# Kernel tuning notes

Measured on AMD Instinct MI355X. Metric: run time of the kernel, lower is better.

## Reference

```python
import jax, jax.numpy as jnp
from jax import lax
import numpy as np

D = 1024   # d_model
N = 64     # d_state
P = 64     # headdim
H = 16     # nheads = d_inner // headdim (d_inner = d_model)
E = 8      # n_experts
R = 8      # LoRA rank
OM = 32    # omega_dim
MEMD = 384 # memory vector dim
KC = 4     # d_conv
Bz, Lz = 2, 1024


def setup_inputs() -> dict:
    key = jax.random.key(0)
    it = iter(jax.random.split(key, 48))
    def nrm(shape, s=0.02):
        return jax.random.normal(next(it), shape, jnp.float32) * s
    return dict(
        x=jax.random.normal(next(it), (Bz, Lz, D), jnp.float32),
        wkv_state=nrm((Bz, N, N), 0.1),
        x_prev=jax.random.normal(next(it), (Bz, 1, D), jnp.float32),
        memory_vec=jax.random.normal(next(it), (Bz, MEMD), jnp.float32),
        rag_state=nrm((Bz, N, N), 0.1),
        ssd_state=nrm((Bz, H, P, N), 0.1),
        conv_state=nrm((Bz, D, KC), 0.1),
        norm_scale=jnp.ones((D,), jnp.float32), norm_bias=jnp.zeros((D,), jnp.float32),
        W_in=nrm((2 * D, D)), conv_w=nrm((D, KC), 0.1), conv_b=jnp.zeros((D,), jnp.float32),
        W_dt=nrm((H, D)), dt_bias=jnp.full((H,), -2.0, jnp.float32),
        A_log=jnp.log(jnp.linspace(0.5, 8.0, H)).astype(jnp.float32),
        W_B=nrm((N, D)), W_C=nrm((N, D)), W_ssd_out=nrm((D, D)),
        W_r=nrm((N, D)), W_k=nrm((N, D)), W_v=nrm((N, D)), W_w=nrm((N, D)),
        W_rwkv_out=nrm((D, N)),
        W_skew=nrm((OM, OM), 0.1), W_om_in=nrm((OM, D)), W_om_out=nrm((D, OM)),
        W_router=nrm((E, D)), lora_A=nrm((E, D, R)), lora_B=nrm((E, R, D)),
        W_nov=nrm((1, 2 * D)), b_nov=jnp.zeros((1,), jnp.float32),
        W_ragq=nrm((N, D)), W_rago=nrm((D, N)),
        W_mq=nrm((MEMD, D)), W_mp=nrm((D, MEMD)),
        W_mg=nrm((1, D + MEMD)), b_mg=jnp.zeros((1,), jnp.float32),
    )


def _layernorm(x, s, b):
    m = x.mean(-1, keepdims=True)
    v = ((x - m) ** 2).mean(-1, keepdims=True)
    return (x - m) * lax.rsqrt(v + 1e-5) * s + b


def _forward(x, wkv_state, x_prev, memory_vec, rag_state, ssd_state, conv_state,
             norm_scale, norm_bias, W_in, conv_w, conv_b, W_dt, dt_bias, A_log,
             W_B, W_C, W_ssd_out, W_r, W_k, W_v, W_w, W_rwkv_out,
             W_skew, W_om_in, W_om_out, W_router, lora_A, lora_B, W_nov, b_nov,
             W_ragq, W_rago, W_mq, W_mp, W_mg, b_mg):
    Bb, Ll, _ = x.shape
    residual = x
    xn = _layernorm(x, norm_scale, norm_bias)
    # ---- TarsCoreBlock: Mamba-2 SSD scan + RWKV-7 wkv scan + gated fusion ----
    zu = xn @ W_in.T
    z, u = zu[..., :D], zu[..., D:]
    # depthwise causal conv1d with rolling conv_state [B, D, KC]
    u_cat = jnp.concatenate([conv_state.transpose(0, 2, 1), u], axis=1)  # [B, KC+L, D]
    acc = conv_b
    for k in range(KC):
        acc = acc + u_cat[:, k:k + Ll, :] * conv_w[:, k]
    uc = jax.nn.silu(acc)
    conv_new = u_cat[:, Ll:, :].transpose(0, 2, 1)
    dt = jax.nn.softplus(xn @ W_dt.T + dt_bias)   # [B,L,H]
    A = -jnp.exp(A_log)                            # [H], negative decay rates
    Bm = xn @ W_B.T                                # [B,L,N]
    Cm = xn @ W_C.T                                # [B,L,N]
    uh = uc.reshape(Bb, Ll, H, P)
    def ssd_step(h, inp):
        dt_t, u_t, b_t, c_t = inp                  # [B,H],[B,H,P],[B,N],[B,N]
        h = h * jnp.exp(dt_t * A)[..., None, None] + (dt_t[..., None, None] * u_t[..., None]) * b_t[:, None, None, :]
        return h, jnp.einsum('bhpn,bn->bhp', h, c_t)
    ssd_new, ys = lax.scan(ssd_step, ssd_state,
                           (dt.transpose(1, 0, 2), uh.transpose(1, 0, 2, 3),
                            Bm.transpose(1, 0, 2), Cm.transpose(1, 0, 2)))
    y_ssd = ys.transpose(1, 0, 2, 3).reshape(Bb, Ll, D) @ W_ssd_out.T
    # RWKV-7 style wkv recurrence with time-shift mixing
    x_shift = jnp.concatenate([x_prev, xn[:, :-1]], axis=1)
    mix = 0.5 * (xn + x_shift)
    r, kk, v = mix @ W_r.T, mix @ W_k.T, mix @ W_v.T
    w = jnp.exp(-jnp.exp(mix @ W_w.T))             # per-channel decay in (0,1)
    def rwkv_step(S, inp):
        r_t, k_t, v_t, w_t = inp
        S = S * w_t[:, :, None] + v_t[:, :, None] * k_t[:, None, :]
        return S, jnp.einsum('bij,bj->bi', S, r_t)
    wkv_new, yr = lax.scan(rwkv_step, wkv_state,
                           (r.transpose(1, 0, 2), kk.transpose(1, 0, 2),
                            v.transpose(1, 0, 2), w.transpose(1, 0, 2)))
    y_rwkv = yr.transpose(1, 0, 2) @ W_rwkv_out.T
    core_out = jax.nn.silu(z) * y_ssd + y_rwkv     # WuNeng fusion
    x1 = residual + core_out
    x_prev_new = xn[:, -1:, :]
    # ---- RAG injection from compressed rag_state ----
    q = x1.mean(1) @ W_ragq.T                      # [B,N]
    info = jnp.einsum('bij,bj->bi', rag_state, q)
    x1 = x1 + 0.1 * (info @ W_rago.T)[:, None, :]
    # ---- Omega-SSM: Cayley SO(n) rotation in omega subspace ----
    Ask = 0.5 * (W_skew - W_skew.T)
    I = jnp.eye(OM, dtype=x.dtype)
    Qc = jnp.linalg.solve(I - Ask, I + Ask)        # orthogonal via Cayley map
    x1 = x1 + ((x1 @ W_om_in.T) @ Qc.T) @ W_om_out.T
    # ---- MoLE: sparse top-2 low-rank (LoRA) experts ----
    probs = jax.nn.softmax(x1 @ W_router.T, axis=-1)  # [B,L,E]
    _, topi = lax.top_k(probs, 2)
    mask = jax.nn.one_hot(topi, E, dtype=x.dtype).sum(-2)
    gate = probs * mask
    gate = gate / (gate.sum(-1, keepdims=True) + 1e-9)
    down = jnp.einsum('bld,edr->bler', x1, lora_A)    # [B,L,E,R]
    x2 = x1 + jnp.einsum('bler,erd->bld', down * gate[..., None], lora_B)
    aux = E * jnp.sum(probs.mean((0, 1)) * mask.mean((0, 1)))
    # ---- NoveltyGate blended residual ----
    h_old, h_new = residual.mean(1), x2.mean(1)
    novelty = jax.nn.sigmoid(jnp.concatenate([h_old, h_new], -1) @ W_nov.T + b_nov)[:, 0]
    n = novelty[:, None, None]
    x3 = n * x2 + (1.0 - n) * residual
    # ---- Cosine-gated memory fusion ----
    h_post = x3.mean(1)
    hq = h_post @ W_mq.T
    sim = (hq * memory_vec).sum(-1) / (jnp.linalg.norm(hq, axis=-1) * jnp.linalg.norm(memory_vec, axis=-1) + 1e-8)
    gm = jax.nn.sigmoid(jnp.concatenate([h_post, memory_vec], -1) @ W_mg.T + b_mg)[:, 0]
    x4 = x3 + (sim * gm)[:, None, None] * (memory_vec @ W_mp.T)[:, None, :]
    return x4, wkv_new, x_prev_new, ssd_new, conv_new, aux


def reference(x, wkv_state, x_prev, memory_vec, rag_state, ssd_state, conv_state,
              norm_scale, norm_bias, W_in, conv_w, conv_b, W_dt, dt_bias, A_log,
              W_B, W_C, W_ssd_out, W_r, W_k, W_v, W_w, W_rwkv_out,
              W_skew, W_om_in, W_om_out, W_router, lora_A, lora_B, W_nov, b_nov,
              W_ragq, W_rago, W_mq, W_mp, W_mg, b_mg):
    return _forward(x, wkv_state, x_prev, memory_vec, rag_state, ssd_state, conv_state,
                    norm_scale, norm_bias, W_in, conv_w, conv_b, W_dt, dt_bias, A_log,
                    W_B, W_C, W_ssd_out, W_r, W_k, W_v, W_w, W_rwkv_out,
                    W_skew, W_om_in, W_om_out, W_router, lora_A, lora_B, W_nov, b_nov,
                    W_ragq, W_rago, W_mq, W_mp, W_mg, b_mg)
```

## Files before the change

### kernel.cpp

```cpp
#include <hip/hip_runtime.h>
#include <hip/hip_bf16.h>

#define DD    1024
#define NN    64
#define HH    16
#define EE    8
#define OMM   32
#define MEMDD 384
#define BB    2
#define LL    1024
#define TT    2048

#define OFF_X4    0
#define OFF_WKV   2097152
#define OFF_XPREV 2105344
#define OFF_SSD   2107392
#define OFF_CONV  2238464
#define OFF_AUX   2246656

typedef unsigned short u16;
typedef __attribute__((ext_vector_type(8))) short short8;
typedef __attribute__((ext_vector_type(4))) float f32x4;

__device__ __forceinline__ float us2f(u16 u){ return __uint_as_float(((unsigned)u)<<16); }
// ... 216 lines not shown
        for (int n=0;n<4;++n) acc[m][n] = (f32x4){0.f,0.f,0.f,0.f};
    for (int k0=0; k0<K; k0+=64){
        #pragma unroll
        for (int i=0;i<2;++i){
            int row = wid*16 + i*8 + lr;
            gl_lds16(Ag + (size_t)row*K + k0 + lc8, &Asm[(wid*16 + i*8)*64]);
        }
        #pragma unroll
        for (int i=0;i<4;++i){
            int row = wid*32 + i*8 + lr;
            gl_lds16(Wg + (size_t)row*K + k0 + lc8, &Bsm[(wid*32 + i*8)*64]);
        }
        __syncthreads();
        #pragma unroll
        for (int ks=0; ks<2; ++ks){
            short8 af[2], bf[4];
            #pragma unroll
            for (int m=0;m<2;++m)
                af[m] = *(const short8*)&Asm[(wr*32 + m*16 + l15)*64 + ks*32 + quad*8];
            #pragma unroll
            for (int n=0;n<4;++n)
                bf[n] = *(const short8*)&Bsm[(wc*64 + n*16 + l15)*64 + ks*32 + quad*8];
            #pragma unroll
            for (int m=0;m<2;++m)
                #pragma unroll
                for (int n=0;n<4;++n)
                    acc[m][n] = __builtin_amdgcn_mfma_f32_16x16x32_bf16(af[m], bf[n], acc[m][n], 0,0,0);
        }
        __syncthreads();
    }
    int ns1 = N - Nsplit;
    #pragma unroll
    for (int m=0;m<2;++m){
        #pragma unroll
        for (int n=0;n<4;++n){
            int col = bn + wc*64 + n*16 + l15;
            #pragma unroll
            for (int i=0;i<4;++i){
                int row = bm + wr*32 + m*16 + quad*4 + i;
                float v = acc[m][n][i];
                if (col < Nsplit){
                    size_t id = (size_t)row*Nsplit + col;
                    if (c0bf) ((u16*)C0)[id] = f2us(v);
                    else C0[id] = (addto ? C0[id] : 0.f) + v;
                } else {
                    size_t id = (size_t)row*ns1 + (col - Nsplit);
                    C1[id] = v;
                }
            }
        }
    }
}

__global__ __launch_bounds__(256)
void gemm_big_k(const u16* __restrict__ A, const u16* __restrict__ W,
                float* __restrict__ C0, float* __restrict__ C1,
                int N, int K, int Nsplit, int addto){
    __shared__ u16 Asm[64*64];
    __shared__ u16 Bsm[128*64];
    gemm_body(Asm, Bsm, A, W, C0, C1, N, K, Nsplit, addto, 0, blockIdx.x, blockIdx.y);
}

__device__ __forceinline__ void gemm64_body(u16* Asm, u16* Bsm,
                const u16* __restrict__ A, const u16* __restrict__ W,
                float* __restrict__ C0, float* __restrict__ C1,
                int N, int K, int Nsplit, int c0bf, int bx, int by){
    int tid = threadIdx.x;
    int wid = tid >> 6, lane = tid & 63;
    int l15 = lane & 15, quad = lane >> 4;
    int wr = wid >> 1, wc = wid & 1;
    int bm = bx*64, bn = by*64;
    int lr = lane >> 3;
    int lc8 = (lane & 7)*8;
    const u16* Ag = A + (size_t)bm*K;
    const u16* Wg = W + (size_t)bn*K;
    f32x4 acc[2][2];
    #pragma unroll
    for (int m=0;m<2;++m)
        #pragma unroll
        for (int n=0;n<2;++n) acc[m][n] = (f32x4){0.f,0.f,0.f,0.f};
    for (int k0=0; k0<K; k0+=64){
        #pragma unroll
        for (int i=0;i<2;++i){
            int row = wid*16 + i*8 + lr;
            gl_lds16(Ag + (size_t)row*K + k0 + lc8, &Asm[(wid*16 + i*8)*64]);
        }
        #pragma unroll
        for (int i=0;i<2;++i){
            int row = wid*16 + i*8 + lr;
            gl_lds16(Wg + (size_t)row*K + k0 + lc8, &Bsm[(wid*16 + i*8)*64]);
        }
        __syncthreads();
        #pragma unroll
        for (int ks=0; ks<2; ++ks){
            short8 af[2], bf[2];
            #pragma unroll
            for (int m=0;m<2;++m)
                af[m] = *(const short8*)&Asm[(wr*32 + m*16 + l15)*64 + ks*32 + quad*8];
            #pragma unroll
            for (int n=0;n<2;++n)
                bf[n] = *(const short8*)&Bsm[(wc*32 + n*16 + l15)*64 + ks*32 + quad*8];
            #pragma unroll
            for (int m=0;m<2;++m)
                #pragma unroll
                for (int n=0;n<2;++n)
                    acc[m][n] = __builtin_amdgcn_mfma_f32_16x16x32_bf16(af[m], bf[n], acc[m][n], 0,0,0);
        }
        __syncthreads();
    }
    int ns1 = N - Nsplit;
    #pragma unroll
    for (int m=0;m<2;++m){
        #pragma unroll
        for (int n=0;n<2;++n){
            int col = bn + wc*32 + n*16 + l15;
// ... 84 lines not shown
                #pragma unroll
                for (int n=0;n<4;++n)
                    acc[m][n] = __builtin_amdgcn_mfma_f32_16x16x32_bf16(af[m], bf[n], acc[m][n], 0,0,0);
        }
        __syncthreads();
    }
    int ns1 = N - Nsplit;
    #pragma unroll
    for (int m=0;m<4;++m){
        #pragma unroll
        for (int n=0;n<4;++n){
            int col = bn + wc*64 + n*16 + l15;
            #pragma unroll
            for (int i=0;i<4;++i){
                int row = bm + wr*64 + m*16 + quad*4 + i;
                float v = acc[m][n][i];
                if (col < Nsplit){
                    C0[(size_t)row*Nsplit + col] = v;
                } else {
                    C1[(size_t)row*ns1 + (col - Nsplit)] = v;
                }
            }
        }
    }
}

__global__ __launch_bounds__(256)
void cmx_k(const float* __restrict__ u, const u16* __restrict__ xnbf,
           const void* __restrict__ cs, const void* __restrict__ cw, const void* __restrict__ cb,
           const void* __restrict__ xprev,
           u16* __restrict__ ucbf, u16* __restrict__ mixbf, void* __restrict__ out,
           const int* modep){
    const int m = *modep;
    int idx = blockIdx.x*256 + threadIdx.x;
    int t = idx >> 10, d = idx & 1023;
    int b = t >> 10, l = t & 1023;
    float acc = LD(cb, d, m);
    #pragma unroll
    for (int k=0;k<4;++k){
        int i = l + k;
        float xv = (i < 4) ? LD(cs, ((size_t)(b*DD + d))*4 + i, m)
                           : u[(size_t)(t + k - 4)*DD + d];
        acc += xv * LD(cw, d*4 + k, m);
    }
    ucbf[idx] = f2us(acc * sigf(acc));
    float xc = us2f(xnbf[idx]);
    float xp = (l == 0) ? LD(xprev, (size_t)b*DD + d, m) : us2f(xnbf[idx - DD]);
    mixbf[idx] = f2us(0.5f*(xc + xp));
    if (l >= LL-4)
        ST(out, OFF_CONV + (size_t)b*DD*4 + d*4 + (l - (LL-4)), u[idx], m);
}

#define LDSS 72
__global__ __launch_bounds__(256)
void ssdA_k(const u16* __restrict__ pcat2, const float* __restrict__ dtraw,
            const u16* __restrict__ ucbf,
            const void* __restrict__ A_log, const void* __restrict__ dt_bias,
            float* __restrict__ ys, float* __restrict__ Scb, float* __restrict__ cumsb,
            const int* modep){
    __shared__ u16 Bs[64*LDSS];
    __shared__ u16 Cs[64*LDSS];
    __shared__ u16 BTw[64*LDSS];
    __shared__ u16 XTs[64*LDSS];
    __shared__ float cums[64];
    __shared__ float dts_raw[64];
    const int m = *modep;
    int tid = threadIdx.x;
    int wid = tid >> 6, lane = tid & 63;
    int blk = blockIdx.x;
    int b = blk >> 8, h = (blk >> 4) & 15, c = blk & 15;
    int l16 = lane & 15, quad = lane >> 4;
    int r = tid >> 2;
    int cb4 = (tid & 3) * 16;
    float Ah = -expf(LD(A_log, h, m));
    int t0 = c*64;
    const u16* Pg = pcat2 + (size_t)(b*LL + t0)*128;
    #pragma unroll
    for (int i=0;i<4;++i){
        int cc = cb4 + i*4;
        ushort4 f = *(const ushort4*)(Pg + (size_t)r*128 + cc);
        u16* d1 = &Bs[r*LDSS + cc];
        d1[0]=f.x; d1[1]=f.y; d1[2]=f.z; d1[3]=f.w;
        ushort4 g = *(const ushort4*)(Pg + (size_t)r*128 + 64 + cc);
        u16* d2 = &Cs[r*LDSS + cc];
        d2[0]=g.x; d2[1]=g.y; d2[2]=g.z; d2[3]=g.w;
    }
    if (wid == 0){
        float raw = dtraw[(size_t)(b*LL + t0 + lane)*128 + h] + LD(dt_bias, h, m);
        float dtv = (raw > 20.f) ? raw : log1pf(expf(raw));
        dts_raw[lane] = dtv;
        float xv = dtv * Ah;
        #pragma unroll
        for (int off=1; off<64; off<<=1){
            float tu = __shfl_up(xv, off);
            if (lane >= off) xv += tu;
        }
        cums[lane] = xv;
        cumsb[(size_t)blk*64 + lane] = xv;
    }
    __syncthreads();
    float cum63 = cums[63];
    {
        float dtv = dts_raw[r];
        float wdec = expf(cum63 - cums[r]);
        const u16* ug = ucbf + (size_t)(b*LL + t0 + r)*DD + h*64;
        #pragma unroll
        for (int i=0;i<4;++i){
            int cc = cb4 + i*4;
            ushort4 f = *(const ushort4*)(ug + cc);
            XTs[(cc+0)*LDSS + r]=f2us(dtv*us2f(f.x));
            XTs[(cc+1)*LDSS + r]=f2us(dtv*us2f(f.y));
            XTs[(cc+2)*LDSS + r]=f2us(dtv*us2f(f.z));
            XTs[(cc+3)*LDSS + r]=f2us(dtv*us2f(f.w));
            u16* bsrc = &Bs[r*LDSS + cc];
            BTw[(cc+0)*LDSS + r] = f2us(us2f(bsrc[0])*wdec);
            BTw[(cc+1)*LDSS + r] = f2us(us2f(bsrc[1])*wdec);
            BTw[(cc+2)*LDSS + r] = f2us(us2f(bsrc[2])*wdec);
            BTw[(cc+3)*LDSS + r] = f2us(us2f(bsrc[3])*wdec);
        }
    }
    __syncthreads();
    f32x4 gacc[4];
    #pragma unroll
    for (int nt=0;nt<4;++nt) gacc[nt]=(f32x4){0.f,0.f,0.f,0.f};
    #pragma unroll
    for (int ks=0; ks<64; ks+=32){
        short8 af = *(const short8*)&Cs[(wid*16 + l16)*LDSS + ks + quad*8];
        #pragma unroll
        for (int nt=0;nt<4;++nt){
            short8 bf = *(const short8*)&Bs[(nt*16 + l16)*LDSS + ks + quad*8];
            gacc[nt] = __builtin_amdgcn_mfma_f32_16x16x32_bf16(af, bf, gacc[nt], 0,0,0);
        }
    }
    __syncthreads();
    #pragma unroll
    for (int nt=0;nt<4;++nt){
        int s_loc = nt*16 + l16;
        #pragma unroll
        for (int i=0;i<4;++i){
            int t_loc = wid*16 + quad*4 + i;
            float gv = (s_loc <= t_loc) ? gacc[nt][i]*expf(cums[t_loc]-cums[s_loc]) : 0.f;
            Bs[t_loc*LDSS + s_loc] = f2us(gv);
        }
    }
    __syncthreads();
    f32x4 acc2[4], acc4[4];
    #pragma unroll
    for (int nt=0;nt<4;++nt){ acc2[nt]=(f32x4){0.f,0.f,0.f,0.f}; acc4[nt]=(f32x4){0.f,0.f,0.f,0.f}; }
    #pragma unroll
    for (int ks=0; ks<64; ks+=32){
        short8 sf = *(const short8*)&Bs[(wid*16 + l16)*LDSS + ks + quad*8];
        short8 xf = *(const short8*)&XTs[(wid*16 + l16)*LDSS + ks + quad*8];
        #pragma unroll
        for (int nt=0;nt<4;++nt){
            short8 xo = *(const short8*)&XTs[(nt*16 + l16)*LDSS + ks + quad*8];
            acc2[nt] = __builtin_amdgcn_mfma_f32_16x16x32_bf16(sf, xo, acc2[nt], 0,0,0);
            short8 bo = *(const short8*)&BTw[(nt*16 + l16)*LDSS + ks + quad*8];
            acc4[nt] = __builtin_amdgcn_mfma_f32_16x16x32_bf16(xf, bo, acc4[nt], 0,0,0);
        }
    }
    #pragma unroll
    for (int nt=0;nt<4;++nt){
        int col = nt*16 + l16;
        #pragma unroll
        for (int i=0;i<4;++i){
            int row = wid*16 + quad*4 + i;
            ys[(size_t)(b*LL + t0 + row)*DD + h*64 + col] = acc2[nt][i];
            Scb[(size_t)blk*4096 + row*64 + col] = acc4[nt][i];
        }
    }
}

#define FS 68
__global__ __launch_bounds__(512)
void rwkvA_k(const float* __restrict__ rkvw,
             float* __restrict__ yr, float* __restrict__ Slb, float* __restrict__ Wcumb){
    __shared__ float wch[64*FS], vch[64*FS], kch[64*FS], rch[64*FS];
    __shared__ float Wc[64*FS];
    __shared__ float part[8*512];
    int tid = threadIdx.x;
    int wid = tid >> 6, lane = tid & 63;
    int blk = blockIdx.x;
    int b = blk >> 4, c = blk & 15;
    int t0 = c*64;
    int r = tid >> 3, c8 = (tid & 7)*8;
    const float* base = rkvw + (size_t)(b*LL + t0)*256;
    #pragma unroll
    for (int i=0;i<2;++i){
        int cc = c8 + i*4;
        *(float4*)&rch[r*FS+cc] = *(const float4*)(base + (size_t)r*256 + cc);
        *(float4*)&kch[r*FS+cc] = *(const float4*)(base + (size_t)r*256 + 64 + cc);
        *(float4*)&vch[r*FS+cc] = *(const float4*)(base + (size_t)r*256 + 128 + cc);
        float4 wv = *(const float4*)(base + (size_t)r*256 + 192 + cc);
        wch[r*FS+cc+0] = expf(-expf(wv.x));
        wch[r*FS+cc+1] = expf(-expf(wv.y));
        wch[r*FS+cc+2] = expf(-expf(wv.z));
        wch[r*FS+cc+3] = expf(-expf(wv.w));
    }
    __syncthreads();
    if (wid == 0){
        float cum = 1.f;
        for (int t=0;t<64;++t){ cum *= wch[t*FS+lane]; Wc[t*FS+lane] = cum; }
    }
    __syncthreads();
    #pragma unroll
    for (int q=0;q<8;++q){
        int idx = q*512 + tid;
        int t = idx >> 6, i = idx & 63;
        Wcumb[(size_t)blk*4096 + idx] = Wc[t*FS + i];
    }
    float S[8];
    #pragma unroll
    for (int jj=0;jj<8;++jj) S[jj]=0.f;
    int jb = wid*8;
    for (int t8=0; t8<8; ++t8){
        float ya[8];
        #pragma unroll
        for (int u=0;u<8;++u){
            int t = t8*8+u;
            float wv = wch[t*FS+lane];
            float vv = vch[t*FS+lane];
            float yy0=0.f, yy1=0.f;
            #pragma unroll
            for (int jj=0;jj<8;jj+=2){
                float k0v = kch[t*FS + jb + jj+0], r0v = rch[t*FS + jb + jj+0];
                float k1v = kch[t*FS + jb + jj+1], r1v = rch[t*FS + jb + jj+1];
                S[jj+0] = S[jj+0]*wv + vv*k0v; yy0 += S[jj+0]*r0v;
                S[jj+1] = S[jj+1]*wv + vv*k1v; yy1 += S[jj+1]*r1v;
            }
            ya[u] = yy0+yy1;
        }
        #pragma unroll
        for (int u=0;u<8;++u) part[wid*512 + u*64 + lane] = ya[u];
        __syncthreads();
        {
            int u = tid >> 6, i = tid & 63;
            float y = 0.f;
            #pragma unroll
            for (int w=0;w<8;++w) y += part[w*512 + u*64 + i];
            yr[(size_t)(b*LL + t0 + t8*8 + u)*NN + i] = y;
        }
        __syncthreads();
    }
    #pragma unroll
    for (int jj=0;jj<8;++jj)
        Slb[(size_t)blk*4096 + (size_t)lane*64 + jb + jj] = S[jj];
}

__global__ __launch_bounds__(256)
void sb_k(const void* __restrict__ ssd_state, const float* __restrict__ Scb,
          const float* __restrict__ cumsb, u16* __restrict__ hinb,
          const void* __restrict__ wkv_state, const float* __restrict__ Slb,
          const float* __restrict__ Wcumb, u16* __restrict__ hinr,
          void* __restrict__ out, const int* modep){
    const int m = *modep;
    int tid = threadIdx.x;
    if (blockIdx.x < 512){
        int bh = blockIdx.x >> 4, i = blockIdx.x & 15;
        int e = i*256 + tid;
        float h = LD(ssd_state, (size_t)bh*4096 + e, m);
        for (int c=0; c<16; ++c){
            int blk = bh*16 + c;
            float efull = expf(cumsb[(size_t)blk*64 + 63]);
            hinb[(size_t)blk*4096 + e] = f2us(h);
            h = efull*h + Scb[(size_t)blk*4096 + e];
        }
        ST(out, OFF_SSD + (size_t)bh*4096 + e, h, m);
    } else {
        int idx2 = blockIdx.x - 512;
        int b = idx2 >> 4, q = idx2 & 15;
        int e = q*256 + tid;
        int i = e >> 6;
        float S = LD(wkv_state, (size_t)b*4096 + e, m);
        for (int c=0; c<16; ++c){
            int blk = b*16 + c;
            hinr[(size_t)blk*4096 + e] = f2us(S);
            float P = Wcumb[(size_t)blk*4096 + 63*64 + i];
            S = S*P + Slb[(size_t)blk*4096 + e];
        }
        ST(out, OFF_WKV + (size_t)b*4096 + e, S, m);
    }
}

__global__ __launch_bounds__(256)
void sc_k(const u16* __restrict__ pcat2, const u16* __restrict__ hinb,
          const float* __restrict__ cumsb, const float* __restrict__ ys, u16* __restrict__ ysbf,
          const float* __restrict__ rkvw, const u16* __restrict__ hinr,
          const float* __restrict__ Wcumb, const float* __restrict__ yr, u16* __restrict__ ybf){
    __shared__ u16 T0[64*LDSS];
    __shared__ u16 T1[64*LDSS];
    int tid = threadIdx.x;
    int wid = tid >> 6, lane = tid & 63;
    int l16 = lane & 15, quad = lane >> 4;
    int r = tid >> 2;
    int cb4 = (tid & 3)*16;
    if (blockIdx.x < 512){
        int blk = blockIdx.x;
        int b = blk >> 8, h = (blk >> 4) & 15, c = blk & 15;
        int t0 = c*64;
// ... 50 lines not shown
        __syncthreads();
        f32x4 acc[4];
        #pragma unroll
        for (int nt=0;nt<4;++nt) acc[nt]=(f32x4){0.f,0.f,0.f,0.f};
        #pragma unroll
        for (int ks=0; ks<64; ks+=32){
            short8 af = *(const short8*)&T0[(wid*16 + l16)*LDSS + ks + quad*8];
            #pragma unroll
            for (int nt=0;nt<4;++nt){
                short8 hf = *(const short8*)&T1[(nt*16 + l16)*LDSS + ks + quad*8];
                acc[nt] = __builtin_amdgcn_mfma_f32_16x16x32_bf16(af, hf, acc[nt], 0,0,0);
            }
        }
        #pragma unroll
        for (int nt=0;nt<4;++nt){
            int col = nt*16 + l16;
            #pragma unroll
            for (int i=0;i<4;++i){
                int row = wid*16 + quad*4 + i;
                float Wt = Wcumb[(size_t)blk*4096 + row*64 + col];
                size_t id = (size_t)(b*LL + t0 + row)*NN + col;
                ybf[id] = f2us(yr[id] + Wt*acc[nt][i]);
            }
        }
    }
}

__global__ __launch_bounds__(256)
void fuse_mean_k(const float* __restrict__ z, const float* __restrict__ s1,
                 const float* __restrict__ s2, const void* __restrict__ xin,
                 float* __restrict__ x1, u16* __restrict__ x1bf, float* __restrict__ mean1,
                 float* __restrict__ hold, const int* modep){
    const int m = *modep;
    int bid = blockIdx.x;
    int lc = bid & 63, dc = (bid >> 6) & 3, b = bid >> 8;
    int d = dc*256 + threadIdx.x;
    float sum = 0.f, sumx = 0.f;
    int l0 = lc*16;
    for (int l=l0; l<l0+16; ++l){
        size_t idx = (size_t)(b*LL + l)*DD + d;
        float zl = z[idx];
        float xv = LD(xin, idx, m);
        float v = xv + zl*sigf(zl)*s1[idx] + s2[idx];
        x1[idx] = v;
        x1bf[idx] = f2us(v);
        sum += v;
        sumx += xv;
    }
    atomicAdd(&mean1[b*DD + d], sum*(1.f/LL));
    atomicAdd(&hold[b*DD + d], sumx*(1.f/LL));
}

__global__ __launch_bounds__(256)
void ragA_k(const float* __restrict__ mean1, const void* __restrict__ W_ragq,
            float* __restrict__ qb, const int* modep){
    const int m = *modep;
    int bx = blockIdx.x;
    int b = bx >> 4;
    int tid = threadIdx.x, wid = tid >> 6, lane = tid & 63;
    int row = (bx & 15)*4 + wid;
    float s = 0.f;
    size_t wo = (size_t)row*DD;
    #pragma unroll
    for (int it=0; it<16; ++it)
        s += LD(W_ragq, wo + it*64 + lane, m) * mean1[(b<<10) + it*64 + lane];
    s = wave_sum64(s);
    if (lane == 0) qb[b*64 + row] = s;
}

__global__ __launch_bounds__(256)
void ragB_k(const float* __restrict__ qb, const void* __restrict__ rag_state,
            float* __restrict__ infob, const int* modep){
    const int m = *modep;
    int bx = blockIdx.x;
    int b = bx >> 4;
    int tid = threadIdx.x, wid = tid >> 6, lane = tid & 63;
    int row = (bx & 15)*4 + wid;
    float s = LD(rag_state, (size_t)(b*64+row)*64 + lane, m) * qb[b*64 + lane];
    s = wave_sum64(s);
    if (lane == 0) infob[b*64 + row] = s;
}

__global__ __launch_bounds__(256)
void ragC_k(const float* __restrict__ infob, const void* __restrict__ W_rago,
            float* __restrict__ ragd, const int* modep){
    const int m = *modep;
    int bx = blockIdx.x;
    int b = bx >> 6;
    int tid = threadIdx.x, wid = tid >> 6, lane = tid & 63;
    int r0 = (bx & 63)*16 + wid*4;
    float iv = infob[b*64 + lane];
    #pragma unroll
    for (int rr=0; rr<4; ++rr){
        int d = r0 + rr;
        float s = iv * LD(W_rago, (size_t)d*64 + lane, m);
        s = wave_sum64(s);
        if (lane == 0) ragd[(b<<10) + d] = 0.1f*s;
    }
}

__global__ __launch_bounds__(256)
void ragV_k(const float* __restrict__ ragd, const u16* __restrict__ wcomb,
            float* __restrict__ rag2v){
    int bx = blockIdx.x;
    int b = bx >> 6;
    int tid = threadIdx.x, wid = tid >> 6, lane = tid & 63;
    int r0 = (bx & 63)*16 + wid*4;
    #pragma unroll
    for (int rr=0; rr<4; ++rr){
        int dp = r0 + rr;
        float s = 0.f;
        #pragma unroll
        for (int it=0; it<16; ++it)
            s += ragd[(b<<10) + it*64 + lane] * us2f(wcomb[(size_t)dp*DD + it*64 + lane]);
        s = wave_sum64(s);
        if (lane == 0) rag2v[(b<<10) + dp] = ragd[(b<<10) + dp] + s;
    }
}

__global__ __launch_bounds__(256)
// ... 257 lines not shown
    float* s2b     = ws + o; o += (size_t)TT*DD;
    float* dtraw   = ws + o; o += (size_t)TT*128;
    float* rkvw    = ws + o; o += (size_t)TT*256;
    float* yrb     = ws + o; o += (size_t)TT*NN;
    float* Qcb     = ws + o; o += 1024;
    float* Scb     = ws + o; o += (size_t)512*4096;
    float* cumsb   = ws + o; o += (size_t)512*64;
    float* Wcumb   = ws + o; o += (size_t)32*4096;
    float* Slb     = ws + o; o += (size_t)32*4096;
    u16*   hinb    = (u16*)(ws + o); o += (size_t)512*4096/2;
    u16*   hinr    = (u16*)(ws + o); o += (size_t)32*4096/2;
    float* mean1   = ws + o; o += BB*DD;
    float* ragd    = ws + o; o += BB*DD;
    float* rag2v   = ws + o; o += BB*DD;
    float* qb      = ws + o; o += BB*NN;
    float* infob   = ws + o; o += BB*NN;
    float* holdb   = ws + o; o += BB*DD;
    float* hnewb   = ws + o; o += BB*DD;
    float* scal    = ws + o; o += 16;
    float* mdel    = ws + o; o += BB*DD;
    float* hqb     = ws + o; o += BB*MEMDD;
    float* probs8  = ws + o; o += (size_t)TT*8;
    int*   eidx    = (int*)(ws + o); o += (size_t)TT*2;
    int*   flag    = (int*)(ws + o); o += 16;
    u16*   xnbf    = (u16*)(ws + o); o += (size_t)TT*DD/2;
    u16*   mixbf   = (u16*)(ws + o); o += (size_t)TT*DD/2;
    u16*   x1bf    = (u16*)(ws + o); o += (size_t)TT*DD/2;
    u16*   ysbf    = (u16*)(ws + o); o += (size_t)TT*DD/2;
    u16*   ucbf    = (u16*)(ws + o); o += (size_t)TT*DD/2;
    u16*   ybf     = (u16*)(ws + o); o += (size_t)TT*NN/2;
    u16*   pcat2   = (u16*)(ws + o); o += (size_t)TT*128/2;
    u16*   wbfin   = (u16*)(ws + o); o += (size_t)2*DD*DD/2;
    u16*   wbfss   = (u16*)(ws + o); o += (size_t)DD*DD/2;
    u16*   wbfrw   = (u16*)(ws + o); o += (size_t)DD*NN/2;
    u16*   wcatxn  = (u16*)(ws + o); o += (size_t)256*DD/2;
    u16*   wcatmix = (u16*)(ws + o); o += (size_t)256*DD/2;
    u16*   wcombbf = (u16*)(ws + o); o += (size_t)DD*DD/2;

    dim3 blk(256);

    hipLaunchKernelGGL(prep_k, dim3(1024,8), blk, 0, stream,
                       nscale, flag, mean1, holdb, hnewb,
                       W_in, wbfin, W_ssd_out, wbfss, W_rwkv_out, wbfrw,
                       W_B, W_C, W_dt, wcatxn, W_r, W_k, W_v, W_w, wcatmix,
                       memv, W_mp, mdel, W_skew, Qcb);
    hipLaunchKernelGGL(ln_k, dim3(TT + 1024), blk, 0, stream, x, nscale, nbias, xnbf, d_out,
                       W_om_out, Qcb, W_om_in, wcombbf, flag);
    hipLaunchKernelGGL(gemm2_k, dim3(TT/128, 16), blk, 0, stream, xnbf, wbfin,
                       z_x2, u_ys, 2*DD, DD, DD);
    hipLaunchKernelGGL(cmx_k, dim3(TT*DD/256), blk, 0, stream, u_ys, xnbf,
                       conv_state, conv_w, conv_b, x_prev, ucbf, mixbf, d_out, flag);
    hipLaunchKernelGGL(proj_dual_k, dim3(TT/64, 8), blk, 0, stream,
                       xnbf, wcatxn, (float*)pcat2, dtraw, mixbf, wcatmix, rkvw);
    hipLaunchKernelGGL(ssdA_k, dim3(512), blk, 0, stream, pcat2, dtraw, ucbf, A_log, dt_bias,
                       u_ys , Scb, cumsb, flag);
    hipLaunchKernelGGL(rwkvA_k, dim3(32), dim3(512), 0, stream, rkvw, yrb, Slb, Wcumb);
    hipLaunchKernelGGL(sb_k, dim3(544), blk, 0, stream, ssd_state, Scb, cumsb, hinb,
                       wkv_state, Slb, Wcumb, hinr, d_out, flag);
    hipLaunchKernelGGL(sc_k, dim3(544), blk, 0, stream, pcat2, hinb, cumsb, u_ys, ysbf,
                       rkvw, hinr, Wcumb, yrb, ybf);
    hipLaunchKernelGGL(out_dual_k, dim3(TT/64, 16), blk, 0, stream,
                       ysbf, wbfss, ucb , ybf, wbfrw, s2b);
    hipLaunchKernelGGL(fuse_mean_k, dim3(512), blk, 0, stream, z_x2, ucb, s2b, x,
                       xn_x1 , x1bf, mean1, holdb, flag);
    hipLaunchKernelGGL(ragA_k, dim3(32), blk, 0, stream, mean1, W_ragq, qb, flag);
    hipLaunchKernelGGL(ragB_k, dim3(32), blk, 0, stream, qb, rag_state, infob, flag);
    hipLaunchKernelGGL(ragC_k, dim3(128), blk, 0, stream, infob, W_rago, ragd, flag);
    hipLaunchKernelGGL(ragV_k, dim3(128), blk, 0, stream, ragd, wcombbf, rag2v);
    hipLaunchKernelGGL(gemm_big_k, dim3(TT/64, 8), blk, 0, stream, x1bf, wcombbf,
                       xn_x1, (float*)nullptr, DD, DD, DD, 1);
    hipLaunchKernelGGL(moe_k, dim3(TT), blk, 0, stream, xn_x1, rag2v, W_router, lora_A, lora_B,
                       z_x2, probs8, eidx, flag);
    hipLaunchKernelGGL(colmean2_k, dim3(512), blk, 0, stream, z_x2, hnewb, flag);
    hipLaunchKernelGGL(hq2_k, dim3(BB,24), blk, 0, stream, holdb, hnewb, W_nov, b_nov,
                       W_mq, hqb, flag);
    hipLaunchKernelGGL(gate2_k, dim3(BB), blk, 0, stream, holdb, hnewb, W_nov, b_nov,
                       hqb, memv, W_mg, b_mg, probs8, eidx, scal, d_out, flag);
    hipLaunchKernelGGL(final_k, dim3(TT*DD/1024), blk, 0, stream, z_x2, x, scal, mdel, d_out, flag);
}
```

Measured before the change: 399.5 us.

## Merge SSD and RWKV chunk kernels and fold ragA into big GEMM launch

Combines the SSD intra-chunk kernel and the RWKV chunk-scan kernel into one 544-block launch whose blocks branch on index, with the RWKV path cut from 512 to 256 threads, each holding 16 state columns. It also folds the small ragA matvec into the x1 GEMM launch as extra blocks. This removes two kernel launches and lets independent small work run alongside larger work instead of serially. In exchange the merged kernel uses a large shared buffer that may lower occupancy, and the RWKV blocks have less parallelism per chunk.

Result: no change. 395.7 us (-0.9%).

```diff
diff --git a/kernel.cpp b/kernel.cpp
--- a/kernel.cpp
+++ b/kernel.cpp
@@ -292,15 +292,6 @@
     }
 }
 
-__global__ __launch_bounds__(256)
-void gemm_big_k(const u16* __restrict__ A, const u16* __restrict__ W,
-                float* __restrict__ C0, float* __restrict__ C1,
-                int N, int K, int Nsplit, int addto){
-    __shared__ u16 Asm[64*64];
-    __shared__ u16 Bsm[128*64];
-    gemm_body(Asm, Bsm, A, W, C0, C1, N, K, Nsplit, addto, 0, blockIdx.x, blockIdx.y);
-}
-
 __device__ __forceinline__ void gemm64_body(u16* Asm, u16* Bsm,
                 const u16* __restrict__ A, const u16* __restrict__ W,
                 float* __restrict__ C0, float* __restrict__ C1,
@@ -491,199 +482,201 @@
 }
 
 #define LDSS 72
-__global__ __launch_bounds__(256)
-void ssdA_k(const u16* __restrict__ pcat2, const float* __restrict__ dtraw,
-            const u16* __restrict__ ucbf,
-            const void* __restrict__ A_log, const void* __restrict__ dt_bias,
-            float* __restrict__ ys, float* __restrict__ Scb, float* __restrict__ cumsb,
-            const int* modep){
-    __shared__ u16 Bs[64*LDSS];
-    __shared__ u16 Cs[64*LDSS];
-    __shared__ u16 BTw[64*LDSS];
-    __shared__ u16 XTs[64*LDSS];
-    __shared__ float cums[64];
-    __shared__ float dts_raw[64];
-    const int m = *modep;
+#define FS 68
+__global__ __launch_bounds__(256)
+void sa_k(const u16* __restrict__ pcat2, const float* __restrict__ dtraw,
+          const u16* __restrict__ ucbf,
+          const void* __restrict__ A_log, const void* __restrict__ dt_bias,
+          float* __restrict__ ys, float* __restrict__ Scb, float* __restrict__ cumsb,
+          const float* __restrict__ rkvw,
+          float* __restrict__ yr, float* __restrict__ Slb, float* __restrict__ Wcumb,
+          const int* modep){
+    __shared__ __align__(16) char smem[77824];
     int tid = threadIdx.x;
     int wid = tid >> 6, lane = tid & 63;
-    int blk = blockIdx.x;
-    int b = blk >> 8, h = (blk >> 4) & 15, c = blk & 15;
-    int l16 = lane & 15, quad = lane >> 4;
-    int r = tid >> 2;
-    int cb4 = (tid & 3) * 16;
-    float Ah = -expf(LD(A_log, h, m));
-    int t0 = c*64;
-    const u16* Pg = pcat2 + (size_t)(b*LL + t0)*128;
-    #pragma unroll
-    for (int i=0;i<4;++i){
-        int cc = cb4 + i*4;
-        ushort4 f = *(const ushort4*)(Pg + (size_t)r*128 + cc);
-        u16* d1 = &Bs[r*LDSS + cc];
-        d1[0]=f.x; d1[1]=f.y; d1[2]=f.z; d1[3]=f.w;
-        ushort4 g = *(const ushort4*)(Pg + (size_t)r*128 + 64 + cc);
-        u16* d2 = &Cs[r*LDSS + cc];
-        d2[0]=g.x; d2[1]=g.y; d2[2]=g.z; d2[3]=g.w;
-    }
-    if (wid == 0){
-        float raw = dtraw[(size_t)(b*LL + t0 + lane)*128 + h] + LD(dt_bias, h, m);
-        float dtv = (raw > 20.f) ? raw : log1pf(expf(raw));
-        dts_raw[lane] = dtv;
-        float xv = dtv * Ah;
-        #pragma unroll
-        for (int off=1; off<64; off<<=1){
-            float tu = __shfl_up(xv, off);
-            if (lane >= off) xv += tu;
-        }
-        cums[lane] = xv;
-        cumsb[(size_t)blk*64 + lane] = xv;
-    }
-    __syncthreads();
-    float cum63 = cums[63];
-    {
-        float dtv = dts_raw[r];
-        float wdec = expf(cum63 - cums[r]);
-        const u16* ug = ucbf + (size_t)(b*LL + t0 + r)*DD + h*64;
+    if (blockIdx.x < 512){
+        u16* Bs  = (u16*)smem;
+        u16* Cs  = Bs  + 64*LDSS;
+        u16* BTw = Cs  + 64*LDSS;
+        u16* XTs = BTw + 64*LDSS;
+        float* cums    = (float*)(XTs + 64*LDSS);
+        float* dts_raw = cums + 64;
+        const int m = *modep;
+        int blk = blockIdx.x;
+        int b = blk >> 8, h = (blk >> 4) & 15, c = blk & 15;
+        int l16 = lane & 15, quad = lane >> 4;
+        int r = tid >> 2;
+        int cb4 = (tid & 3) * 16;
+        float Ah = -expf(LD(A_log, h, m));
+        int t0 = c*64;
+        const u16* Pg = pcat2 + (size_t)(b*LL + t0)*128;
         #pragma unroll
         for (int i=0;i<4;++i){
             int cc = cb4 + i*4;
-            ushort4 f = *(const ushort4*)(ug + cc);
-            XTs[(cc+0)*LDSS + r]=f2us(dtv*us2f(f.x));
-            XTs[(cc+1)*LDSS + r]=f2us(dtv*us2f(f.y));
-            XTs[(cc+2)*LDSS + r]=f2us(dtv*us2f(f.z));
-            XTs[(cc+3)*LDSS + r]=f2us(dtv*us2f(f.w));
-            u16* bsrc = &Bs[r*LDSS + cc];
-            BTw[(cc+0)*LDSS + r] = f2us(us2f(bsrc[0])*wdec);
-            BTw[(cc+1)*LDSS + r] = f2us(us2f(bsrc[1])*wdec);
-            BTw[(cc+2)*LDSS + r] = f2us(us2f(bsrc[2])*wdec);
-            BTw[(cc+3)*LDSS + r] = f2us(us2f(bsrc[3])*wdec);
-        }
-    }
-    __syncthreads();
-    f32x4 gacc[4];
-    #pragma unroll
-    for (int nt=0;nt<4;++nt) gacc[nt]=(f32x4){0.f,0.f,0.f,0.f};
-    #pragma unroll
-    for (int ks=0; ks<64; ks+=32){
-        short8 af = *(const short8*)&Cs[(wid*16 + l16)*LDSS + ks + quad*8];
+            ushort4 f = *(const ushort4*)(Pg + (size_t)r*128 + cc);
+            u16* d1 = &Bs[r*LDSS + cc];
+            d1[0]=f.x; d1[1]=f.y; d1[2]=f.z; d1[3]=f.w;
+            ushort4 g = *(const ushort4*)(Pg + (size_t)r*128 + 64 + cc);
+            u16* d2 = &Cs[r*LDSS + cc];
+            d2[0]=g.x; d2[1]=g.y; d2[2]=g.z; d2[3]=g.w;
+        }
+        if (wid == 0){
+            float raw = dtraw[(size_t)(b*LL + t0 + lane)*128 + h] + LD(dt_bias, h, m);
+            float dtv = (raw > 20.f) ? raw : log1pf(expf(raw));
+            dts_raw[lane] = dtv;
+            float xv = dtv * Ah;
+            #pragma unroll
+            for (int off=1; off<64; off<<=1){
+                float tu = __shfl_up(xv, off);
+                if (lane >= off) xv += tu;
+            }
+            cums[lane] = xv;
+            cumsb[(size_t)blk*64 + lane] = xv;
+        }
+        __syncthreads();
+        float cum63 = cums[63];
+        {
+            float dtv = dts_raw[r];
+            float wdec = expf(cum63 - cums[r]);
+            const u16* ug = ucbf + (size_t)(b*LL + t0 + r)*DD + h*64;
+            #pragma unroll
+            for (int i=0;i<4;++i){
+                int cc = cb4 + i*4;
+                ushort4 f = *(const ushort4*)(ug + cc);
+                XTs[(cc+0)*LDSS + r]=f2us(dtv*us2f(f.x));
+                XTs[(cc+1)*LDSS + r]=f2us(dtv*us2f(f.y));
+                XTs[(cc+2)*LDSS + r]=f2us(dtv*us2f(f.z));
+                XTs[(cc+3)*LDSS + r]=f2us(dtv*us2f(f.w));
+                u16* bsrc = &Bs[r*LDSS + cc];
+                BTw[(cc+0)*LDSS + r] = f2us(us2f(bsrc[0])*wdec);
+                BTw[(cc+1)*LDSS + r] = f2us(us2f(bsrc[1])*wdec);
+                BTw[(cc+2)*LDSS + r] = f2us(us2f(bsrc[2])*wdec);
+                BTw[(cc+3)*LDSS + r] = f2us(us2f(bsrc[3])*wdec);
+            }
+        }
+        __syncthreads();
+        f32x4 gacc[4];
+        #pragma unroll
+        for (int nt=0;nt<4;++nt) gacc[nt]=(f32x4){0.f,0.f,0.f,0.f};
+        #pragma unroll
+        for (int ks=0; ks<64; ks+=32){
+            short8 af = *(const short8*)&Cs[(wid*16 + l16)*LDSS + ks + quad*8];
+            #pragma unroll
+            for (int nt=0;nt<4;++nt){
+                short8 bf = *(const short8*)&Bs[(nt*16 + l16)*LDSS + ks + quad*8];
+                gacc[nt] = __builtin_amdgcn_mfma_f32_16x16x32_bf16(af, bf, gacc[nt], 0,0,0);
+            }
+        }
+        __syncthreads();
         #pragma unroll
         for (int nt=0;nt<4;++nt){
-            short8 bf = *(const short8*)&Bs[(nt*16 + l16)*LDSS + ks + quad*8];
-            gacc[nt] = __builtin_amdgcn_mfma_f32_16x16x32_bf16(af, bf, gacc[nt], 0,0,0);
-        }
-    }
-    __syncthreads();
-    #pragma unroll
-    for (int nt=0;nt<4;++nt){
-        int s_loc = nt*16 + l16;
+            int s_loc = nt*16 + l16;
+            #pragma unroll
+            for (int i=0;i<4;++i){
+                int t_loc = wid*16 + quad*4 + i;
+                float gv = (s_loc <= t_loc) ? gacc[nt][i]*expf(cums[t_loc]-cums[s_loc]) : 0.f;
+                Bs[t_loc*LDSS + s_loc] = f2us(gv);
+            }
+        }
+        __syncthreads();
+        f32x4 acc2[4], acc4[4];
+        #pragma unroll
+        for (int nt=0;nt<4;++nt){ acc2[nt]=(f32x4){0.f,0.f,0.f,0.f}; acc4[nt]=(f32x4){0.f,0.f,0.f,0.f}; }
+        #pragma unroll
+        for (int ks=0; ks<64; ks+=32){
+            short8 sf = *(const short8*)&Bs[(wid*16 + l16)*LDSS + ks + quad*8];
+            short8 xf = *(const short8*)&XTs[(wid*16 + l16)*LDSS + ks + quad*8];
+            #pragma unroll
+            for (int nt=0;nt<4;++nt){
+                short8 xo = *(const short8*)&XTs[(nt*16 + l16)*LDSS + ks + quad*8];
+                acc2[nt] = __builtin_amdgcn_mfma_f32_16x16x32_bf16(sf, xo, acc2[nt], 0,0,0);
+                short8 bo = *(const short8*)&BTw[(nt*16 + l16)*LDSS + ks + quad*8];
+                acc4[nt] = __builtin_amdgcn_mfma_f32_16x16x32_bf16(xf, bo, acc4[nt], 0,0,0);
+            }
+        }
+        #pragma unroll
+        for (int nt=0;nt<4;++nt){
+            int col = nt*16 + l16;
+            #pragma unroll
+            for (int i=0;i<4;++i){
+                int row = wid*16 + quad*4 + i;
+                ys[(size_t)(b*LL + t0 + row)*DD + h*64 + col] = acc2[nt][i];
+                Scb[(size_t)blk*4096 + row*64 + col] = acc4[nt][i];
+            }
+        }
+    } else {
+        float* wch = (float*)smem;
+        float* vch = wch + 64*FS;
+        float* kch = vch + 64*FS;
+        float* rch = kch + 64*FS;
+        float* part = rch + 64*FS;
+        int blk = blockIdx.x - 512;
+        int b = blk >> 4, c = blk & 15;
+        int t0 = c*64;
+        int r = tid >> 2, c4 = (tid & 3)*16;
+        const float* base = rkvw + (size_t)(b*LL + t0)*256;
         #pragma unroll
         for (int i=0;i<4;++i){
-            int t_loc = wid*16 + quad*4 + i;
-            float gv = (s_loc <= t_loc) ? gacc[nt][i]*expf(cums[t_loc]-cums[s_loc]) : 0.f;
-            Bs[t_loc*LDSS + s_loc] = f2us(gv);
-        }
-    }
-    __syncthreads();
-    f32x4 acc2[4], acc4[4];
-    #pragma unroll
-    for (int nt=0;nt<4;++nt){ acc2[nt]=(f32x4){0.f,0.f,0.f,0.f}; acc4[nt]=(f32x4){0.f,0.f,0.f,0.f}; }
-    #pragma unroll
-    for (int ks=0; ks<64; ks+=32){
-        short8 sf = *(const short8*)&Bs[(wid*16 + l16)*LDSS + ks + quad*8];
-        short8 xf = *(const short8*)&XTs[(wid*16 + l16)*LDSS + ks + quad*8];
-        #pragma unroll
-        for (int nt=0;nt<4;++nt){
-            short8 xo = *(const short8*)&XTs[(nt*16 + l16)*LDSS + ks + quad*8];
-            acc2[nt] = __builtin_amdgcn_mfma_f32_16x16x32_bf16(sf, xo, acc2[nt], 0,0,0);
-            short8 bo = *(const short8*)&BTw[(nt*16 + l16)*LDSS + ks + quad*8];
-            acc4[nt] = __builtin_amdgcn_mfma_f32_16x16x32_bf16(xf, bo, acc4[nt], 0,0,0);
-        }
-    }
-    #pragma unroll
-    for (int nt=0;nt<4;++nt){
-        int col = nt*16 + l16;
-        #pragma unroll
-        for (int i=0;i<4;++i){
-            int row = wid*16 + quad*4 + i;
-            ys[(size_t)(b*LL + t0 + row)*DD + h*64 + col] = acc2[nt][i];
-            Scb[(size_t)blk*4096 + row*64 + col] = acc4[nt][i];
-        }
-    }
-}
-
-#define FS 68
-__global__ __launch_bounds__(512)
-void rwkvA_k(const float* __restrict__ rkvw,
-             float* __restrict__ yr, float* __restrict__ Slb, float* __restrict__ Wcumb){
-    __shared__ float wch[64*FS], vch[64*FS], kch[64*FS], rch[64*FS];
-    __shared__ float Wc[64*FS];
-    __shared__ float part[8*512];
-    int tid = threadIdx.x;
-    int wid = tid >> 6, lane = tid & 63;
-    int blk = blockIdx.x;
-    int b = blk >> 4, c = blk & 15;
-    int t0 = c*64;
-    int r = tid >> 3, c8 = (tid & 7)*8;
-    const float* base = rkvw + (size_t)(b*LL + t0)*256;
-    #pragma unroll
-    for (int i=0;i<2;++i){
-        int cc = c8 + i*4;
-        *(float4*)&rch[r*FS+cc] = *(const float4*)(base + (size_t)r*256 + cc);
-        *(float4*)&kch[r*FS+cc] = *(const float4*)(base + (size_t)r*256 + 64 + cc);
-        *(float4*)&vch[r*FS+cc] = *(const float4*)(base + (size_t)r*256 + 128 + cc);
-        float4 wv = *(const float4*)(base + (size_t)r*256 + 192 + cc);
-        wch[r*FS+cc+0] = expf(-expf(wv.x));
-        wch[r*FS+cc+1] = expf(-expf(wv.y));
-        wch[r*FS+cc+2] = expf(-expf(wv.z));
-        wch[r*FS+cc+3] = expf(-expf(wv.w));
-    }
-    __syncthreads();
-    if (wid == 0){
-        float cum = 1.f;
-        for (int t=0;t<64;++t){ cum *= wch[t*FS+lane]; Wc[t*FS+lane] = cum; }
-    }
-    __syncthreads();
-    #pragma unroll
-    for (int q=0;q<8;++q){
-        int idx = q*512 + tid;
-        int t = idx >> 6, i = idx & 63;
-        Wcumb[(size_t)blk*4096 + idx] = Wc[t*FS + i];
-    }
-    float S[8];
-    #pragma unroll
-    for (int jj=0;jj<8;++jj) S[jj]=0.f;
-    int jb = wid*8;
-    for (int t8=0; t8<8; ++t8){
-        float ya[8];
-        #pragma unroll
-        for (int u=0;u<8;++u){
-            int t = t8*8+u;
-            float wv = wch[t*FS+lane];
-            float vv = vch[t*FS+lane];
-            float yy0=0.f, yy1=0.f;
-            #pragma unroll
-            for (int jj=0;jj<8;jj+=2){
-                float k0v = kch[t*FS + jb + jj+0], r0v = rch[t*FS + jb + jj+0];
-                float k1v = kch[t*FS + jb + jj+1], r1v = rch[t*FS + jb + jj+1];
-                S[jj+0] = S[jj+0]*wv + vv*k0v; yy0 += S[jj+0]*r0v;
-                S[jj+1] = S[jj+1]*wv + vv*k1v; yy1 += S[jj+1]*r1v;
-            }
-            ya[u] = yy0+yy1;
-        }
-        #pragma unroll
-        for (int u=0;u<8;++u) part[wid*512 + u*64 + lane] = ya[u];
-        __syncthreads();
-        {
-            int u = tid >> 6, i = tid & 63;
-            float y = 0.f;
-            #pragma unroll
-            for (int w=0;w<8;++w) y += part[w*512 + u*64 + i];
-            yr[(size_t)(b*LL + t0 + t8*8 + u)*NN + i] = y;
-        }
-        __syncthreads();
-    }
-    #pragma unroll
-    for (int jj=0;jj<8;++jj)
-        Slb[(size_t)blk*4096 + (size_t)lane*64 + jb + jj] = S[jj];
+            int cc = c4 + i*4;
+            *(float4*)&rch[r*FS+cc] = *(const float4*)(base + (size_t)r*256 + cc);
+            *(float4*)&kch[r*FS+cc] = *(const float4*)(base + (size_t)r*256 + 64 + cc);
+            *(float4*)&vch[r*FS+cc] = *(const float4*)(base + (size_t)r*256 + 128 + cc);
+            float4 wv = *(const float4*)(base + (size_t)r*256 + 192 + cc);
+            wch[r*FS+cc+0] = expf(-expf(wv.x));
+            wch[r*FS+cc+1] = expf(-expf(wv.y));
+            wch[r*FS+cc+2] = expf(-expf(wv.z));
+            wch[r*FS+cc+3] = expf(-expf(wv.w));
+        }
+        __syncthreads();
+        if (wid == 0){
+            float cum = 1.f;
+            for (int t=0;t<64;++t){
+                cum *= wch[t*FS+lane];
+                Wcumb[(size_t)blk*4096 + t*64 + lane] = cum;
+            }
+        }
+        float S[16];
+        #pragma unroll
+        for (int jj=0;jj<16;++jj) S[jj]=0.f;
+        int jb = wid*16;
+        for (int t8=0; t8<8; ++t8){
+            float ya[8];
+            #pragma unroll
+            for (int u=0;u<8;++u){
+                int t = t8*8+u;
+                float wv = wch[t*FS+lane];
+                float vv = vch[t*FS+lane];
+                float yy0=0.f, yy1=0.f, yy2=0.f, yy3=0.f;
+                #pragma unroll
+                for (int jj=0;jj<16;jj+=4){
+                    float k0v = kch[t*FS + jb + jj+0], r0v = rch[t*FS + jb + jj+0];
+                    float k1v = kch[t*FS + jb + jj+1], r1v = rch[t*FS + jb + jj+1];
+                    float k2v = kch[t*FS + jb + jj+2], r2v = rch[t*FS + jb + jj+2];
+                    float k3v = kch[t*FS + jb + jj+3], r3v = rch[t*FS + jb + jj+3];
+                    S[jj+0] = S[jj+0]*wv + vv*k0v; yy0 += S[jj+0]*r0v;
+                    S[jj+1] = S[jj+1]*wv + vv*k1v; yy1 += S[jj+1]*r1v;
+                    S[jj+2] = S[jj+2]*wv + vv*k2v; yy2 += S[jj+2]*r2v;
+                    S[jj+3] = S[jj+3]*wv + vv*k3v; yy3 += S[jj+3]*r3v;
+                }
+                ya[u] = (yy0+yy1)+(yy2+yy3);
+            }
+            #pragma unroll
+            for (int u=0;u<8;++u) part[wid*512 + u*64 + lane] = ya[u];
+            __syncthreads();
+            #pragma unroll
+            for (int it=0; it<2; ++it){
+                int e = it*256 + tid;
+                int u = e >> 6, i = e & 63;
+                float y = part[0*512 + u*64 + i] + part[1*512 + u*64 + i]
+                        + part[2*512 + u*64 + i] + part[3*512 + u*64 + i];
+                yr[(size_t)(b*LL + t0 + t8*8 + u)*NN + i] = y;
+            }
+            __syncthreads();
+        }
+        #pragma unroll
+        for (int jj=0;jj<16;++jj)
+            Slb[(size_t)blk*4096 + (size_t)lane*64 + jb + jj] = S[jj];
+    }
 }
 
 __global__ __launch_bounds__(256)
@@ -840,20 +833,29 @@
 }
 
 __global__ __launch_bounds__(256)
-void ragA_k(const float* __restrict__ mean1, const void* __restrict__ W_ragq,
-            float* __restrict__ qb, const int* modep){
-    const int m = *modep;
-    int bx = blockIdx.x;
-    int b = bx >> 4;
-    int tid = threadIdx.x, wid = tid >> 6, lane = tid & 63;
-    int row = (bx & 15)*4 + wid;
-    float s = 0.f;
-    size_t wo = (size_t)row*DD;
-    #pragma unroll
-    for (int it=0; it<16; ++it)
-        s += LD(W_ragq, wo + it*64 + lane, m) * mean1[(b<<10) + it*64 + lane];
-    s = wave_sum64(s);
-    if (lane == 0) qb[b*64 + row] = s;
+void omrag_k(const u16* __restrict__ x1bf, const u16* __restrict__ wcombbf,
+             float* __restrict__ x1,
+             const float* __restrict__ mean1, const void* __restrict__ W_ragq,
+             float* __restrict__ qb, const int* modep){
+    __shared__ u16 Asm[64*64];
+    __shared__ u16 Bsm[128*64];
+    if (blockIdx.x < 256){
+        gemm_body(Asm, Bsm, x1bf, wcombbf, x1, (float*)nullptr, DD, DD, DD, 1, 0,
+                  blockIdx.x & 31, blockIdx.x >> 5);
+    } else {
+        const int m = *modep;
+        int bx = blockIdx.x - 256;
+        int b = bx >> 4;
+        int tid = threadIdx.x, wid = tid >> 6, lane = tid & 63;
+        int row = (bx & 15)*4 + wid;
+        float s = 0.f;
+        size_t wo = (size_t)row*DD;
+        #pragma unroll
+        for (int it=0; it<16; ++it)
+            s += LD(W_ragq, wo + it*64 + lane, m) * mean1[(b<<10) + it*64 + lane];
+        s = wave_sum64(s);
+        if (lane == 0) qb[b*64 + row] = s;
+    }
 }
 
 __global__ __launch_bounds__(256)
@@ -1217,9 +1219,8 @@
                        conv_state, conv_w, conv_b, x_prev, ucbf, mixbf, d_out, flag);
     hipLaunchKernelGGL(proj_dual_k, dim3(TT/64, 8), blk, 0, stream,
                        xnbf, wcatxn, (float*)pcat2, dtraw, mixbf, wcatmix, rkvw);
-    hipLaunchKernelGGL(ssdA_k, dim3(512), blk, 0, stream, pcat2, dtraw, ucbf, A_log, dt_bias,
-                       u_ys , Scb, cumsb, flag);
-    hipLaunchKernelGGL(rwkvA_k, dim3(32), dim3(512), 0, stream, rkvw, yrb, Slb, Wcumb);
+    hipLaunchKernelGGL(sa_k, dim3(544), blk, 0, stream, pcat2, dtraw, ucbf, A_log, dt_bias,
+                       u_ys , Scb, cumsb, rkvw, yrb, Slb, Wcumb, flag);
     hipLaunchKernelGGL(sb_k, dim3(544), blk, 0, stream, ssd_state, Scb, cumsb, hinb,
                        wkv_state, Slb, Wcumb, hinr, d_out, flag);
     hipLaunchKernelGGL(sc_k, dim3(544), blk, 0, stream, pcat2, hinb, cumsb, u_ys, ysbf,
@@ -1228,12 +1229,11 @@
                        ysbf, wbfss, ucb , ybf, wbfrw, s2b);
     hipLaunchKernelGGL(fuse_mean_k, dim3(512), blk, 0, stream, z_x2, ucb, s2b, x,
                        xn_x1 , x1bf, mean1, holdb, flag);
-    hipLaunchKernelGGL(ragA_k, dim3(32), blk, 0, stream, mean1, W_ragq, qb, flag);
+    hipLaunchKernelGGL(omrag_k, dim3(288), blk, 0, stream, x1bf, wcombbf, xn_x1,
+                       mean1, W_ragq, qb, flag);
     hipLaunchKernelGGL(ragB_k, dim3(32), blk, 0, stream, qb, rag_state, infob, flag);
     hipLaunchKernelGGL(ragC_k, dim3(128), blk, 0, stream, infob, W_rago, ragd, flag);
     hipLaunchKernelGGL(ragV_k, dim3(128), blk, 0, stream, ragd, wcombbf, rag2v);
-    hipLaunchKernelGGL(gemm_big_k, dim3(TT/64, 8), blk, 0, stream, x1bf, wcombbf,
-                       xn_x1, (float*)nullptr, DD, DD, DD, 1);
     hipLaunchKernelGGL(moe_k, dim3(TT), blk, 0, stream, xn_x1, rag2v, W_router, lora_A, lora_B,
                        z_x2, probs8, eidx, flag);
     hipLaunchKernelGGL(colmean2_k, dim3(512), blk, 0, stream, z_x2, hnewb, flag);
```
